# Performance work log

Measured on AMD Instinct MI355X. Metric: run time of the kernel, lower is better.

The kernel has to match this reference:

```python
import jax, jax.numpy as jnp
import numpy as np

N, E, C = 20000, 320000, 10000
IN, H, D = 768, 8, 64
HD = H * D
SA_H = 128


def _gat(feat, src, dst, W, al, ar, b):
    # DGL GATConv: fc -> per-node attn terms -> edge leaky_relu -> edge softmax over dst -> scatter-add -> bias -> elu
    h = (feat @ W).reshape(N, H, D)                       # [N,H,D]
    el = (h * al).sum(-1)                                 # [N,H]
    er = (h * ar).sum(-1)                                 # [N,H]
    e = jax.nn.leaky_relu(el[src] + er[dst], 0.2)         # [E,H]
    m = jax.ops.segment_max(e, dst, num_segments=N)       # [N,H]
    m = jnp.where(jnp.isfinite(m), m, 0.0)                # zero in-degree nodes
    ee = jnp.exp(e - m[dst])                              # [E,H]
    denom = jax.ops.segment_sum(ee, dst, num_segments=N)  # [N,H]
    a = ee / jnp.maximum(denom[dst], 1e-9)                # [E,H]
    out = jax.ops.segment_sum(a[:, :, None] * h[src], dst, num_segments=N)  # [N,H,D]
    return jax.nn.elu(out + b.reshape(1, H, D))


def _sem(z, w1, b1, w2):
    # SemanticAttention: per-metapath score -> softmax over metapaths -> weighted sum
    w = (jnp.tanh(z @ w1 + b1) @ w2).mean(0)              # [M,1]
    beta = jax.nn.softmax(w, axis=0)                      # [M,1]
    return (beta[None] * z).sum(1)                        # [C,HD]


def setup_inputs():
    key = jax.random.key(0)
    ks = jax.random.split(key, 32)
    inp = {}
    for i in range(3):
        inp[f"feat{i}"] = jax.random.normal(ks[i], (N, IN), jnp.float32)
        inp[f"src{i}"] = jax.random.randint(ks[3 + i], (E,), 0, N, dtype=jnp.int32)
        inp[f"dst{i}"] = jax.random.randint(ks[6 + i], (E,), 0, N, dtype=jnp.int32)
        inp[f"char{i}"] = jnp.arange(C, dtype=jnp.int32)
        inp[f"W{i}"] = jax.random.normal(ks[9 + i], (IN, HD), jnp.float32) * 0.05
        inp[f"al{i}"] = jax.random.normal(ks[12 + i], (H, D), jnp.float32) * 0.05
        inp[f"ar{i}"] = jax.random.normal(ks[15 + i], (H, D), jnp.float32) * 0.05
        inp[f"b{i}"] = jnp.zeros((HD,), jnp.float32)
    inp["sw1"] = jax.random.normal(ks[18], (HD, SA_H), jnp.float32) * 0.05
    inp["sb1"] = jnp.zeros((SA_H,), jnp.float32)
    inp["sw2"] = jax.random.normal(ks[19], (SA_H, 1), jnp.float32) * 0.05
    inp["aw1"] = jax.random.normal(ks[20], (HD, SA_H), jnp.float32) * 0.05
    inp["ab1"] = jnp.zeros((SA_H,), jnp.float32)
    inp["aw2"] = jax.random.normal(ks[21], (SA_H, 1), jnp.float32) * 0.05
    return inp


def reference(feat0, feat1, feat2, src0, src1, src2, dst0, dst1, dst2, char0, char1, char2,
              W0, W1, W2, al0, al1, al2, ar0, ar1, ar2, b0, b1, b2,
              sw1, sb1, sw2, aw1, ab1, aw2):
    h1 = _gat(feat0, src0, dst0, W0, al0, ar0, b0)        # [N,H,D]
    hh = _gat(feat2, src2, dst2, W2, al2, ar2, b2)        # [N,H,D]
    z = jnp.stack([h1[char0].reshape(C, HD), hh[char2].reshape(C, HD)], axis=1)  # [C,2,HD]
    sound = _sem(z, sw1, sb1, sw2)                        # [C,HD]
    h2 = _gat(feat1, src1, dst1, W1, al1, ar1, b1)        # [N,H,D]
    z2 = jnp.stack([sound, h2[char1].reshape(C, HD)], axis=1)  # [C,2,HD]
    sem_emb = _sem(z2, aw1, ab1, aw2).reshape(C, H, D)    # [C,H,D]
    h1 = h1.at[char0].set(sem_emb)
    h2 = h2.at[char1].set(sem_emb)
    hh = hh.at[char2].set(sem_emb)
    return sem_emb, h1.mean(1), h2.mean(1), hh.mean(1)
```

## Files before the change

kernel.cpp:

```cpp
#include <hip/hip_runtime.h>
#include <math.h>

#define NN 20000
#define NE 320000
#define CC 10000
#define KIN 768
#define NH 8
#define ND 64
#define NHD 512
#define NSA 128
#define NBKT 79

#define WTB_SZ (NHD * KIN)
#define W1TB_SZ (NSA * NHD)

typedef __attribute__((ext_vector_type(4))) float f32x4;
typedef __attribute__((ext_vector_type(8))) short s16x8;

__device__ __forceinline__ unsigned short f2bf(float f) {
  unsigned u = __float_as_uint(f);
  u += 0x7fffu + ((u >> 16) & 1u);
  return (unsigned short)(u >> 16);
}
__device__ __forceinline__ float bf2f(unsigned short s) {
  return __uint_as_float(((unsigned)s) << 16);
}
__device__ __forceinline__ float bflo(unsigned u) { return __uint_as_float(u << 16); }
__device__ __forceinline__ float bfhi(unsigned u) { return __uint_as_float(u & 0xffff0000u); }

__device__ __forceinline__ void gl_lds16(const void* g, void* l) {
  __builtin_amdgcn_global_load_lds(
      (const __attribute__((address_space(1))) unsigned int*)g,
      (__attribute__((address_space(3))) unsigned int*)l, 16, 0, 0);
}

__global__ void k_prep(const float* __restrict__ W0, const float* __restrict__ W1,
                       const float* __restrict__ W2, const float* __restrict__ sw1,
                       const float* __restrict__ aw1, unsigned short* __restrict__ wtb3,
                       unsigned short* __restrict__ w1tb2, int* __restrict__ deg3,
                       float* __restrict__ scal) {
  int i = blockIdx.x * 256 + threadIdx.x;
  if (i < 3 * WTB_SZ) {
    int g = i / WTB_SZ;
    int j = i - g * WTB_SZ;
    int n = j / KIN, k = j - n * KIN;
    const float* W = (g == 0) ? W0 : (g == 1) ? W1 : W2;
    wtb3[i] = f2bf(W[(size_t)k * NHD + n]);
    return;
  }
  i -= 3 * WTB_SZ;
  if (i < 2 * W1TB_SZ) {
    int p = i / W1TB_SZ;
    int j = i - p * W1TB_SZ;
    int n = j / NHD, k = j - n * NHD;
    const float* W = p ? aw1 : sw1;
    w1tb2[p * W1TB_SZ + n * NHD + k] = f2bf(W[(size_t)k * NSA + n]);
    return;
  }
  i -= 2 * W1TB_SZ;
  if (i < 3 * NN) { deg3[i] = 0; return; }
  i -= 3 * NN;
  if (i < 4) scal[i] = 0.f;
}

__global__ void k_cast_feat(const float* __restrict__ s, unsigned short* __restrict__ d, int n4) {
  int i = blockIdx.x * 256 + threadIdx.x;
  if (i >= n4) return;
  float4 v = ((const float4*)s)[i];
  ushort4 o;
  o.x = f2bf(v.x); o.y = f2bf(v.y); o.z = f2bf(v.z); o.w = f2bf(v.w);
  ((ushort4*)d)[i] = o;
}

template <int OUTBF>
__global__ __launch_bounds__(256, 2) void k_gemm(const unsigned short* __restrict__ A,
                                                 const unsigned short* __restrict__ Bt,
                                                 float* __restrict__ outf,
                                                 unsigned short* __restrict__ outb,
                                                 int M, int K, int ldc) {
  __shared__ unsigned short As[128 * 32];
  __shared__ unsigned short Bs[128 * 32];
  const int tid = threadIdx.x;
  const int wv = tid >> 6, lane = tid & 63;
  const int row0 = blockIdx.x * 128;
  const int col0 = blockIdx.y * 128;
  const int wr = (wv >> 1) * 64, wc = (wv & 1) * 64;
  const int ci = lane & 3, rsub = lane >> 2;

  f32x4 acc[4][4] = {};

  const int l15 = lane & 15;
  const int pc = (((lane >> 4) ^ ((l15 >> 1) & 3))) * 8;

  for (int k0 = 0; k0 < K; k0 += 32) {
#pragma unroll
    for (int i = 0; i < 2; i++) {
      int lrow = (wv * 2 + i) * 16 + rsub;
      int kc = (ci ^ ((lrow >> 1) & 3)) << 3;
      int ga = row0 + lrow; if (ga > M - 1) ga = M - 1;
      gl_lds16(A + (size_t)ga * K + k0 + kc, As + (wv * 2 + i) * 512);
      int gb = col0 + lrow;
      gl_lds16(Bt + (size_t)gb * K + k0 + kc, Bs + (wv * 2 + i) * 512);
    }
    __syncthreads();
    s16x8 af[4], bf[4];
#pragma unroll
    for (int m = 0; m < 4; m++) {
      af[m] = *(const s16x8*)(As + (wr + m * 16 + l15) * 32 + pc);
      bf[m] = *(const s16x8*)(Bs + (wc + m * 16 + l15) * 32 + pc);
    }
#pragma unroll
    for (int m = 0; m < 4; m++)
#pragma unroll
      for (int n = 0; n < 4; n++)
        acc[m][n] = __builtin_amdgcn_mfma_f32_16x16x32_bf16(af[m], bf[n], acc[m][n], 0, 0, 0);
    __syncthreads();
  }

  const int cbase = col0 + wc + l15;
  const int rq = (lane >> 4) * 4;
#pragma unroll
  for (int m = 0; m < 4; m++) {
#pragma unroll
    for (int r = 0; r < 4; r++) {
      int grow = row0 + wr + m * 16 + rq + r;
      if (grow < M) {
        if (OUTBF) {
          unsigned short* dp = outb + (size_t)grow * ldc + cbase;
#pragma unroll
          for (int n = 0; n < 4; n++) dp[n * 16] = f2bf(acc[m][n][r]);
        } else {
          float* dp = outf + (size_t)grow * ldc + cbase;
#pragma unroll
          for (int n = 0; n < 4; n++) dp[n * 16] = acc[m][n][r];
        }
      }
    }
  }
}

__global__ __launch_bounds__(256, 2) void k_gemm_sem(const unsigned short* __restrict__ A,
                                                     const unsigned short* __restrict__ Bt,
                                                     const float* __restrict__ b1,
                                                     const float* __restrict__ w2,
                                                     float* __restrict__ scal,
                                                     int M, int K) {
  __shared__ unsigned short As[128 * 32];
  __shared__ unsigned short Bs[128 * 32];
  __shared__ float rsum[2][128];
  __shared__ float pp[2][2];
  const int tid = threadIdx.x;
  const int wv = tid >> 6, lane = tid & 63;
  const int row0 = blockIdx.x * 128;
  const int wr = (wv >> 1) * 64, wc = (wv & 1) * 64;
  const int ci = lane & 3, rsub = lane >> 2;

  f32x4 acc[4][4] = {};

  const int l15 = lane & 15;
  const int pc = (((lane >> 4) ^ ((l15 >> 1) & 3))) * 8;

  for (int k0 = 0; k0 < K; k0 += 32) {
#pragma unroll
    for (int i = 0; i < 2; i++) {
      int lrow = (wv * 2 + i) * 16 + rsub;
      int kc = (ci ^ ((lrow >> 1) & 3)) << 3;
      int ga = row0 + lrow; if (ga > M - 1) ga = M - 1;
      gl_lds16(A + (size_t)ga * K + k0 + kc, As + (wv * 2 + i) * 512);
      int gb = lrow;
      gl_lds16(Bt + (size_t)gb * K + k0 + kc, Bs + (wv * 2 + i) * 512);
    }
    __syncthreads();
    s16x8 af[4], bf[4];
#pragma unroll
    for (int m = 0; m < 4; m++) {
      af[m] = *(const s16x8*)(As + (wr + m * 16 + l15) * 32 + pc);
      bf[m] = *(const s16x8*)(Bs + (wc + m * 16 + l15) * 32 + pc);
    }
#pragma unroll
    for (int m = 0; m < 4; m++)
#pragma unroll
      for (int n = 0; n < 4; n++)
        acc[m][n] = __builtin_amdgcn_mfma_f32_16x16x32_bf16(af[m], bf[n], acc[m][n], 0, 0, 0);
    __syncthreads();
  }

  if (tid < 128) { rsum[0][tid] = 0.f; rsum[1][tid] = 0.f; }
  __syncthreads();
  const int cb = wc + l15;
  const int rq = (lane >> 4) * 4;
  float b1c[4], w2c[4];
#pragma unroll
  for (int n = 0; n < 4; n++) { b1c[n] = b1[cb + n * 16]; w2c[n] = w2[cb + n * 16]; }
#pragma unroll
  for (int m = 0; m < 4; m++) {
#pragma unroll
    for (int r = 0; r < 4; r++) {
      int rl = wr + m * 16 + rq + r;
      float s = 0.f;
#pragma unroll
      for (int n = 0; n < 4; n++) s += tanhf(acc[m][n][r] + b1c[n]) * w2c[n];
      s += __shfl_xor(s, 1, 64); s += __shfl_xor(s, 2, 64);
      s += __shfl_xor(s, 4, 64); s += __shfl_xor(s, 8, 64);
      if (l15 == 0 && row0 + rl < M) rsum[wv & 1][rl] = s;
    }
  }
  __syncthreads();
  if (tid < 128) {
    int grow = row0 + tid;
    float v = rsum[0][tid] + rsum[1][tid];
    float vA = (grow < CC) ? v : 0.f;
    float vB = (grow >= CC && grow < M) ? v : 0.f;
#pragma unroll
    for (int off = 32; off > 0; off >>= 1) {
      vA += __shfl_xor(vA, off, 64);
      vB += __shfl_xor(vB, off, 64);
    }
    if ((tid & 63) == 0) { pp[tid >> 6][0] = vA; pp[tid >> 6][1] = vB; }
  }
  __syncthreads();
  if (tid == 0) {
    atomicAdd(scal + 0, pp[0][0] + pp[1][0]);
    atomicAdd(scal + 1, pp[0][1] + pp[1][1]);
  }
}

__global__ void k_elr(const unsigned short* __restrict__ hb, const float* __restrict__ al,
                      const float* __restrict__ ar, float* __restrict__ el,
                      float* __restrict__ er) {
  int t = (blockIdx.x * 256 + threadIdx.x) >> 6;
  int lane = threadIdx.x & 63;
  uint4 hv = *(const uint4*)(hb + (size_t)t * NHD + lane * 8);
  float4 al0 = ((const float4*)(al + lane * 8))[0];
  float4 al1 = ((const float4*)(al + lane * 8))[1];
  float4 ar0 = ((const float4*)(ar + lane * 8))[0];
  float4 ar1 = ((const float4*)(ar + lane * 8))[1];
  float h0 = bflo(hv.x), h1 = bfhi(hv.x), h2 = bflo(hv.y), h3 = bfhi(hv.y);
  float h4 = bflo(hv.z), h5 = bfhi(hv.z), h6 = bflo(hv.w), h7 = bfhi(hv.w);
  float a = h0 * al0.x + h1 * al0.y + h2 * al0.z + h3 * al0.w +
            h4 * al1.x + h5 * al1.y + h6 * al1.z + h7 * al1.w;
  float b = h0 * ar0.x + h1 * ar0.y + h2 * ar0.z + h3 * ar0.w +
            h4 * ar1.x + h5 * ar1.y + h6 * ar1.z + h7 * ar1.w;
#pragma unroll
  for (int off = 1; off < 8; off <<= 1) {
    a += __shfl_xor(a, off, 64);
    b += __shfl_xor(b, off, 64);
  }
  if ((lane & 7) == 0) {
    el[(size_t)t * NH + (lane >> 3)] = a;
    er[(size_t)t * NH + (lane >> 3)] = b;
  }
}

__global__ void k_hist3(const int* __restrict__ d0, const int* __restrict__ d1,
                        const int* __restrict__ d2, int* __restrict__ deg3) {
  int e = blockIdx.x * 256 + threadIdx.x;
  int g = blockIdx.y;
  const int* dst = (g == 0) ? d0 : (g == 1) ? d1 : d2;
  atomicAdd(deg3 + g * NN + dst[e], 1);
}

__global__ __launch_bounds__(1024) void k_scan3(const int* __restrict__ deg3,
                                                int* __restrict__ rowptr3,
                                                int* __restrict__ curB) {
  __shared__ int part[1024];
  const int g = blockIdx.x;
  const int* deg = deg3 + g * NN;
  int* rowptr = rowptr3 + g * (NN + 1);
  int tid = threadIdx.x;
  const int CH = 20;
  int base = tid * CH;
  int s = 0;
  for (int i = 0; i < CH; i++) { int idx = base + i; if (idx < NN) s += deg[idx]; }
  part[tid] = s;
  __syncthreads();
  for (int off = 1; off < 1024; off <<= 1) {
    int u = (tid >= off) ? part[tid - off] : 0;
    int v = part[tid];
    __syncthreads();
    part[tid] = u + v;
    __syncthreads();
  }
  int run = (tid == 0) ? 0 : part[tid - 1];
  for (int i = 0; i < CH; i++) {
    int idx = base + i;
    if (idx < NN) {
      rowptr[idx] = run;
      if ((idx & 255) == 0) curB[g * (NBKT + 1) + (idx >> 8)] = run;
      run += deg[idx];
    }
  }
  if (tid == 1023) rowptr[NN] = part[1023];
}

__global__ __launch_bounds__(1024) void k_coarse(const int* __restrict__ s0,
                                                 const int* __restrict__ s1,
                                                 const int* __restrict__ s2,
                                                 const int* __restrict__ d0,
                                                 const int* __restrict__ d1,
                                                 const int* __restrict__ d2,
                                                 int* __restrict__ curB,
                                                 unsigned* __restrict__ staging) {
  __shared__ int bcnt[NBKT];
  __shared__ int bbase[NBKT];
  int g = blockIdx.y;
  const int* src = (g == 0) ? s0 : (g == 1) ? s1 : s2;
  const int* dst = (g == 0) ? d0 : (g == 1) ? d1 : d2;
  int tid = threadIdx.x;
  if (tid < NBKT) bcnt[tid] = 0;
  __syncthreads();
  int e = blockIdx.x * 1024 + tid;
  bool val = e < NE;
  int b = 0, r = 0, sv = 0, dv = 0;
  if (val) {
    dv = dst[e]; sv = src[e];
    b = dv >> 8;
    r = atomicAdd(&bcnt[b], 1);
  }
  __syncthreads();
  if (tid < NBKT && bcnt[tid] > 0) bbase[tid] = atomicAdd(&curB[g * (NBKT + 1) + tid], bcnt[tid]);
  __syncthreads();
  if (val) staging[(size_t)g * NE + bbase[b] + r] = ((unsigned)sv << 8) | (unsigned)(dv & 255);
}

__global__ __launch_bounds__(1024) void k_fine(const int* __restrict__ rowptr3,
                                               const unsigned* __restrict__ staging,
                                               unsigned short* __restrict__ srcord3) {
  __shared__ int cur[256];
  int g = blockIdx.y, b = blockIdx.x;
  const int* rowptr = rowptr3 + g * (NN + 1);
  int n0 = b << 8;
  int tid = threadIdx.x;
  if (tid < 256) {
    int node = n0 + tid;
    cur[tid] = (node < NN) ? rowptr[node] : 0;
  }
  __syncthreads();
  int nend = n0 + 256; if (nend > NN) nend = NN;
  int start = rowptr[n0];
  int endp = rowptr[nend];
  for (int i = start + tid; i < endp; i += 1024) {
    unsigned u = staging[(size_t)g * NE + i];
    int nl = u & 255;
    int pos = atomicAdd(&cur[nl], 1);
    srcord3[(size_t)g * NE + pos] = (unsigned short)(u >> 8);
  }
}

__global__ __launch_bounds__(256) void k_aggf(const int* __restrict__ rowptr,
                                              const unsigned short* __restrict__ srcord,
                                              const float* __restrict__ el,
                                              const float* __restrict__ er,
                                              const unsigned short* __restrict__ hb,
                                              const float* __restrict__ bias,
                                              float* __restrict__ o,
                                              unsigned short* __restrict__ zb) {
  __shared__ float aS[4][64 * 8];
  __shared__ int sS[4][64];
  int wv = threadIdx.x >> 6;
  int t = (blockIdx.x * 256 + threadIdx.x) >> 6;
  int lane = threadIdx.x & 63;
  int h = lane >> 3;
  int beg = rowptr[t], end = rowptr[t + 1];

  float4 er0 = ((const float4*)(er + (size_t)t * NH))[0];
  float4 er1 = ((const float4*)(er + (size_t)t * NH))[1];
  float erow[8] = {er0.x, er0.y, er0.z, er0.w, er1.x, er1.y, er1.z, er1.w};

  float acc[8] = {0.f, 0.f, 0.f, 0.f, 0.f, 0.f, 0.f, 0.f};
  float den = 0.f;

  for (int cbeg = beg; cbeg < end; cbeg += 64) {
    int cnt = end - cbeg; if (cnt > 64) cnt = 64;
    bool valid = lane < cnt;
    int pidx = cbeg + lane; if (pidx > end - 1) pidx = end - 1;
    int s = srcord[pidx];
    if (valid) {
      sS[wv][lane] = s;
      float4 a0 = ((const float4*)(el + (size_t)s * NH))[0];
      float4 a1 = ((const float4*)(el + (size_t)s * NH))[1];
      float v[8] = {a0.x + erow[0], a0.y + erow[1], a0.z + erow[2], a0.w + erow[3],
                    a1.x + erow[4], a1.y + erow[5], a1.z + erow[6], a1.w + erow[7]};
#pragma unroll
      for (int k = 0; k < 8; k++) {
        float x = v[k];
        x = x >= 0.f ? x : 0.2f * x;
        aS[wv][lane * 8 + k] = expf(x);
      }
    }
    const unsigned short* hbl = hb + lane * 8;
    int q = 0;
    for (; q + 1 < cnt; q += 2) {
      int s0 = sS[wv][q], s1 = sS[wv][q + 1];
      float w0 = aS[wv][q * 8 + h];
      float w1 = aS[wv][(q + 1) * 8 + h];
      uint4 v0 = *(const uint4*)(hbl + (size_t)s0 * NHD);
      uint4 v1 = *(const uint4*)(hbl + (size_t)s1 * NHD);
      den += w0 + w1;
      acc[0] += w0 * bflo(v0.x); acc[1] += w0 * bfhi(v0.x);
      acc[2] += w0 * bflo(v0.y); acc[3] += w0 * bfhi(v0.y);
      acc[4] += w0 * bflo(v0.z); acc[5] += w0 * bfhi(v0.z);
      acc[6] += w0 * bflo(v0.w); acc[7] += w0 * bfhi(v0.w);
      acc[0] += w1 * bflo(v1.x); acc[1] += w1 * bfhi(v1.x);
      acc[2] += w1 * bflo(v1.y); acc[3] += w1 * bfhi(v1.y);
      acc[4] += w1 * bflo(v1.z); acc[5] += w1 * bfhi(v1.z);
      acc[6] += w1 * bflo(v1.w); acc[7] += w1 * bfhi(v1.w);
    }
    if (q < cnt) {
      int s0 = sS[wv][q];
      float w0 = aS[wv][q * 8 + h];
      uint4 v0 = *(const uint4*)(hbl + (size_t)s0 * NHD);
      den += w0;
      acc[0] += w0 * bflo(v0.x); acc[1] += w0 * bfhi(v0.x);
      acc[2] += w0 * bflo(v0.y); acc[3] += w0 * bfhi(v0.y);
      acc[4] += w0 * bflo(v0.z); acc[5] += w0 * bfhi(v0.z);
      acc[6] += w0 * bflo(v0.w); acc[7] += w0 * bfhi(v0.w);
    }
  }

  float dn = 1.f / fmaxf(den, 1e-9f);
  float4 b0 = ((const float4*)(bias + lane * 8))[0];
  float4 b1 = ((const float4*)(bias + lane * 8))[1];
  float r[8];
  r[0] = acc[0] * dn + b0.x; r[1] = acc[1] * dn + b0.y;
  r[2] = acc[2] * dn + b0.z; r[3] = acc[3] * dn + b0.w;
  r[4] = acc[4] * dn + b1.x; r[5] = acc[5] * dn + b1.y;
  r[6] = acc[6] * dn + b1.z; r[7] = acc[7] * dn + b1.w;
#pragma unroll
  for (int j = 0; j < 8; j++) r[j] = r[j] > 0.f ? r[j] : expm1f(r[j]);
  float* op = o + (size_t)t * NHD + lane * 8;
  ((float4*)op)[0] = make_float4(r[0], r[1], r[2], r[3]);
  ((float4*)op)[1] = make_float4(r[4], r[5], r[6], r[7]);
  if (t < CC) {
    uint4 z;
    z.x = ((unsigned)f2bf(r[1]) << 16) | f2bf(r[0]);
    z.y = ((unsigned)f2bf(r[3]) << 16) | f2bf(r[2]);
    z.z = ((unsigned)f2bf(r[5]) << 16) | f2bf(r[4]);
    z.w = ((unsigned)f2bf(r[7]) << 16) | f2bf(r[6]);
    *(uint4*)(zb + (size_t)t * NHD + lane * 8) = z;
  }
}

__global__ void k_combine_s1(const float* __restrict__ scal, const float* __restrict__ zA,
                             const float* __restrict__ zB, unsigned short* __restrict__ outb) {
  int i = blockIdx.x * 256 + threadIdx.x;
  float w0 = scal[0] * (1.f / CC), w1v = scal[1] * (1.f / CC);
  float mx = fmaxf(w0, w1v);
  float e0 = expf(w0 - mx), e1 = expf(w1v - mx);
  float inv = 1.f / (e0 + e1);
  float b0 = e0 * inv, b1v = e1 * inv;
  float4 a = ((const float4*)zA)[i];
  float4 b = ((const float4*)zB)[i];
  ushort4 z;
  z.x = f2bf(b0 * a.x + b1v * b.x);
  z.y = f2bf(b0 * a.y + b1v * b.y);
  z.z = f2bf(b0 * a.z + b1v * b.z);
  z.w = f2bf(b0 * a.w + b1v * b.w);
  ((ushort4*)outb)[i] = z;
}

__global__ void k_comb2_means(const float* __restrict__ scal,
                              const unsigned short* __restrict__ zsound,
                              const float* __restrict__ o0, const float* __restrict__ o1,
                              const float* __restrict__ o2, float* __restrict__ outf,
                              float* __restrict__ m1, float* __restrict__ m2,
                              float* __restrict__ m3) {
  int idx = blockIdx.x * 256 + threadIdx.x;
  int n = idx >> 6, d = idx & 63;
  if (n < CC) {
    float w0 = scal[0] * (1.f / CC), w1v = scal[1] * (1.f / CC);
    float mx = fmaxf(w0, w1v);
    float e0 = expf(w0 - mx), e1 = expf(w1v - mx);
    float inv = 1.f / (e0 + e1);
    float b0 = e0 * inv, b1v = e1 * inv;
    const unsigned short* zs = zsound + (size_t)n * NHD + d;
    const float* p1 = o1 + (size_t)n * NHD + d;
    float* po = outf + (size_t)n * NHD + d;
    float v = 0.f;
#pragma unroll
    for (int h = 0; h < 8; h++) {
      float r = b0 * bf2f(zs[h * 64]) + b1v * p1[h * 64];
      po[h * 64] = r;
      v += r;
    }
    v *= 0.125f;
    m1[idx] = v; m2[idx] = v; m3[idx] = v;
  } else {
    const float* p0 = o0 + (size_t)n * NHD + d;
    const float* p1 = o1 + (size_t)n * NHD + d;
    const float* p2 = o2 + (size_t)n * NHD + d;
    float v0 = 0.f, v1 = 0.f, v2 = 0.f;
#pragma unroll
    for (int h = 0; h < 8; h++) { v0 += p0[h * 64]; v1 += p1[h * 64]; v2 += p2[h * 64]; }
    m1[idx] = v0 * 0.125f; m2[idx] = v1 * 0.125f; m3[idx] = v2 * 0.125f;
  }
}

extern "C" void kernel_launch(void* const* d_in, const int* in_sizes, int n_in,
                              void* d_out, int out_size, void* d_ws, size_t ws_size,
                              hipStream_t stream) {
  (void)in_sizes; (void)n_in; (void)out_size; (void)ws_size;

  const float* feat[3]; const int* srcp[3]; const int* dstp[3];
  const float* Wp[3]; const float* alp[3]; const float* arp[3]; const float* bp[3];
  for (int g = 0; g < 3; g++) {
    const int base = g * 8;
    feat[g] = (const float*)d_in[base + 0];
    srcp[g] = (const int*)d_in[base + 1];
    dstp[g] = (const int*)d_in[base + 2];
    Wp[g]   = (const float*)d_in[base + 4];
    alp[g]  = (const float*)d_in[base + 5];
    arp[g]  = (const float*)d_in[base + 6];
    bp[g]   = (const float*)d_in[base + 7];
  }
  const float* sw1 = (const float*)d_in[24];
  const float* sb1 = (const float*)d_in[25];
  const float* sw2 = (const float*)d_in[26];
  const float* aw1 = (const float*)d_in[27];
  const float* ab1 = (const float*)d_in[28];
  const float* aw2 = (const float*)d_in[29];

  char* wsp = (char*)d_ws;
  auto alloc = [&](size_t bytes) {
    char* p = wsp;
    wsp += (bytes + 255) & ~(size_t)255;
    return p;
  };
  float* o0 = (float*)alloc((size_t)NN * NHD * 4);
  float* o1 = (float*)alloc((size_t)NN * NHD * 4);
  float* o2 = (float*)alloc((size_t)NN * NHD * 4);
  unsigned short* hb = (unsigned short*)alloc((size_t)NN * NHD * 2);
  unsigned short* featb = (unsigned short*)alloc((size_t)NN * KIN * 2);
  unsigned short* wtb3 = (unsigned short*)alloc((size_t)3 * WTB_SZ * 2);
  unsigned short* w1tb2 = (unsigned short*)alloc((size_t)2 * W1TB_SZ * 2);
  unsigned short* zcat = (unsigned short*)alloc((size_t)2 * CC * NHD * 2);
  float* el = (float*)alloc((size_t)NN * NH * 4);
  float* er = (float*)alloc((size_t)NN * NH * 4);
  float* scal = (float*)alloc(256);
  int* deg3 = (int*)alloc((size_t)3 * NN * 4);
  int* rowptr3 = (int*)alloc((size_t)3 * (NN + 1) * 4 + 64);
  int* curB = (int*)alloc((size_t)3 * (NBKT + 1) * 4);
  unsigned* staging = (unsigned*)alloc((size_t)3 * NE * 4);
  unsigned short* srcord3 = (unsigned short*)alloc((size_t)3 * NE * 2);

  float* outf = (float*)d_out;
  float* outm1 = outf + (size_t)CC * NHD;
  float* outm2 = outm1 + (size_t)NN * ND;
  float* outm3 = outm2 + (size_t)NN * ND;

  const int PREP_T = 3 * WTB_SZ + 2 * W1TB_SZ + 3 * NN + 4;
  k_prep<<<(PREP_T + 255) / 256, 256, 0, stream>>>(Wp[0], Wp[1], Wp[2], sw1, aw1,
                                                   wtb3, w1tb2, deg3, scal);
  k_hist3<<<dim3(NE / 256, 3), 256, 0, stream>>>(dstp[0], dstp[1], dstp[2], deg3);
  k_scan3<<<3, 1024, 0, stream>>>(deg3, rowptr3, curB);
  k_coarse<<<dim3((NE + 1023) / 1024, 3), 1024, 0, stream>>>(
      srcp[0], srcp[1], srcp[2], dstp[0], dstp[1], dstp[2], curB, staging);
  k_fine<<<dim3(NBKT, 3), 1024, 0, stream>>>(rowptr3, staging, srcord3);

  auto gat = [&](int g, float* og, unsigned short* zb) {
    k_cast_feat<<<NN * KIN / 4 / 256, 256, 0, stream>>>(feat[g], featb, NN * KIN / 4);
    k_gemm<1><<<dim3((NN + 127) / 128, NHD / 128), 256, 0, stream>>>(
        featb, wtb3 + (size_t)g * WTB_SZ, nullptr, hb, NN, KIN, NHD);
    k_elr<<<NN * 64 / 256, 256, 0, stream>>>(hb, alp[g], arp[g], el, er);
    k_aggf<<<NN * 64 / 256, 256, 0, stream>>>(rowptr3 + g * (NN + 1), srcord3 + (size_t)g * NE,
                                              el, er, hb, bp[g], og, zb);
  };

  gat(0, o0, zcat);
  gat(2, o2, zcat + (size_t)CC * NHD);

  k_gemm_sem<<<(2 * CC + 127) / 128, 256, 0, stream>>>(zcat, w1tb2, sb1, sw2, scal, 2 * CC, NHD);
  k_combine_s1<<<CC * NHD / 4 / 256, 256, 0, stream>>>(scal, o0, o2, zcat);

  gat(1, o1, zcat + (size_t)CC * NHD);

  k_gemm_sem<<<(2 * CC + 127) / 128, 256, 0, stream>>>(zcat, w1tb2 + W1TB_SZ, ab1, aw2,
                                                       scal + 2, 2 * CC, NHD);
  k_comb2_means<<<NN * 64 / 256, 256, 0, stream>>>(scal + 2, zcat, o0, o1, o2,
                                                   outf, outm1, outm2, outm3);
}
```

Before: 492.7 us.

## Fuse attention logits into GEMM epilogue and split aggregation per head

The GEMM epilogue now computes per-head el/er dot products with wave shuffles and writes them in a head-major layout, which removes the separate k_elr pass that re-read h. The aggregation kernel is restructured so each wave handles one (node, head) pair: it computes a single attention weight per edge and processes eight edges in parallel across lane groups, then reduces with shuffles. Blocks interleave heads so that gathers of the same source row are spread over eight blocks. This costs eight times more waves, repeated rowptr and srcord reads per head, and a cross-lane reduction at the end.

```diff
diff --git a/kernel.cpp b/kernel.cpp
--- a/kernel.cpp
+++ b/kernel.cpp
@@ -72,12 +72,13 @@
   ((ushort4*)d)[i] = o;
 }
 
-template <int OUTBF>
-__global__ __launch_bounds__(256, 2) void k_gemm(const unsigned short* __restrict__ A,
-                                                 const unsigned short* __restrict__ Bt,
-                                                 float* __restrict__ outf,
-                                                 unsigned short* __restrict__ outb,
-                                                 int M, int K, int ldc) {
+__global__ __launch_bounds__(256, 2) void k_gemm_gat(const unsigned short* __restrict__ A,
+                                                     const unsigned short* __restrict__ Bt,
+                                                     unsigned short* __restrict__ outb,
+                                                     const float* __restrict__ al,
+                                                     const float* __restrict__ ar,
+                                                     float* __restrict__ el_t,
+                                                     float* __restrict__ er_t) {
   __shared__ unsigned short As[128 * 32];
   __shared__ unsigned short Bs[128 * 32];
   const int tid = threadIdx.x;
@@ -92,15 +93,15 @@
   const int l15 = lane & 15;
   const int pc = (((lane >> 4) ^ ((l15 >> 1) & 3))) * 8;
 
-  for (int k0 = 0; k0 < K; k0 += 32) {
+  for (int k0 = 0; k0 < KIN; k0 += 32) {
 #pragma unroll
     for (int i = 0; i < 2; i++) {
       int lrow = (wv * 2 + i) * 16 + rsub;
       int kc = (ci ^ ((lrow >> 1) & 3)) << 3;
-      int ga = row0 + lrow; if (ga > M - 1) ga = M - 1;
-      gl_lds16(A + (size_t)ga * K + k0 + kc, As + (wv * 2 + i) * 512);
+      int ga = row0 + lrow; if (ga > NN - 1) ga = NN - 1;
+      gl_lds16(A + (size_t)ga * KIN + k0 + kc, As + (wv * 2 + i) * 512);
       int gb = col0 + lrow;
-      gl_lds16(Bt + (size_t)gb * K + k0 + kc, Bs + (wv * 2 + i) * 512);
+      gl_lds16(Bt + (size_t)gb * KIN + k0 + kc, Bs + (wv * 2 + i) * 512);
     }
     __syncthreads();
     s16x8 af[4], bf[4];
@@ -119,20 +120,34 @@
 
   const int cbase = col0 + wc + l15;
   const int rq = (lane >> 4) * 4;
+  const int hd = (col0 + wc) >> 6;
+  float alc[4], arc[4];
+#pragma unroll
+  for (int n = 0; n < 4; n++) { alc[n] = al[cbase + n * 16]; arc[n] = ar[cbase + n * 16]; }
+
 #pragma unroll
   for (int m = 0; m < 4; m++) {
 #pragma unroll
     for (int r = 0; r < 4; r++) {
       int grow = row0 + wr + m * 16 + rq + r;
-      if (grow < M) {
-        if (OUTBF) {
-          unsigned short* dp = outb + (size_t)grow * ldc + cbase;
-#pragma unroll
-          for (int n = 0; n < 4; n++) dp[n * 16] = f2bf(acc[m][n][r]);
-        } else {
-          float* dp = outf + (size_t)grow * ldc + cbase;
-#pragma unroll
-          for (int n = 0; n < 4; n++) dp[n * 16] = acc[m][n][r];
+      float a = 0.f, b = 0.f;
+#pragma unroll
+      for (int n = 0; n < 4; n++) {
+        float v = acc[m][n][r];
+        a += v * alc[n];
+        b += v * arc[n];
+      }
+      a += __shfl_xor(a, 1, 64); a += __shfl_xor(a, 2, 64);
+      a += __shfl_xor(a, 4, 64); a += __shfl_xor(a, 8, 64);
+      b += __shfl_xor(b, 1, 64); b += __shfl_xor(b, 2, 64);
+      b += __shfl_xor(b, 4, 64); b += __shfl_xor(b, 8, 64);
+      if (grow < NN) {
+        unsigned short* dp = outb + (size_t)grow * NHD + cbase;
+#pragma unroll
+        for (int n = 0; n < 4; n++) dp[n * 16] = f2bf(acc[m][n][r]);
+        if (l15 == 0) {
+          el_t[hd * NN + grow] = a;
+          er_t[hd * NN + grow] = b;
         }
       }
     }
@@ -225,33 +240,6 @@
   }
 }
 
-__global__ void k_elr(const unsigned short* __restrict__ hb, const float* __restrict__ al,
-                      const float* __restrict__ ar, float* __restrict__ el,
-                      float* __restrict__ er) {
-  int t = (blockIdx.x * 256 + threadIdx.x) >> 6;
-  int lane = threadIdx.x & 63;
-  uint4 hv = *(const uint4*)(hb + (size_t)t * NHD + lane * 8);
-  float4 al0 = ((const float4*)(al + lane * 8))[0];
-  float4 al1 = ((const float4*)(al + lane * 8))[1];
-  float4 ar0 = ((const float4*)(ar + lane * 8))[0];
-  float4 ar1 = ((const float4*)(ar + lane * 8))[1];
-  float h0 = bflo(hv.x), h1 = bfhi(hv.x), h2 = bflo(hv.y), h3 = bfhi(hv.y);
-  float h4 = bflo(hv.z), h5 = bfhi(hv.z), h6 = bflo(hv.w), h7 = bfhi(hv.w);
-  float a = h0 * al0.x + h1 * al0.y + h2 * al0.z + h3 * al0.w +
-            h4 * al1.x + h5 * al1.y + h6 * al1.z + h7 * al1.w;
-  float b = h0 * ar0.x + h1 * ar0.y + h2 * ar0.z + h3 * ar0.w +
-            h4 * ar1.x + h5 * ar1.y + h6 * ar1.z + h7 * ar1.w;
-#pragma unroll
-  for (int off = 1; off < 8; off <<= 1) {
-    a += __shfl_xor(a, off, 64);
-    b += __shfl_xor(b, off, 64);
-  }
-  if ((lane & 7) == 0) {
-    el[(size_t)t * NH + (lane >> 3)] = a;
-    er[(size_t)t * NH + (lane >> 3)] = b;
-  }
-}
-
 __global__ void k_hist3(const int* __restrict__ d0, const int* __restrict__ d1,
                         const int* __restrict__ d2, int* __restrict__ deg3) {
   int e = blockIdx.x * 256 + threadIdx.x;
@@ -347,97 +335,86 @@
   }
 }
 
-__global__ __launch_bounds__(256) void k_aggf(const int* __restrict__ rowptr,
+__global__ __launch_bounds__(256) void k_aggs(const int* __restrict__ rowptr,
                                               const unsigned short* __restrict__ srcord,
-                                              const float* __restrict__ el,
-                                              const float* __restrict__ er,
+                                              const float* __restrict__ el_t,
+                                              const float* __restrict__ er_t,
                                               const unsigned short* __restrict__ hb,
                                               const float* __restrict__ bias,
                                               float* __restrict__ o,
                                               unsigned short* __restrict__ zb) {
-  __shared__ float aS[4][64 * 8];
-  __shared__ int sS[4][64];
+  __shared__ float aS[4][64];
+  __shared__ unsigned short sS[4][64];
+  int bid = blockIdx.x;
+  int s = bid & 7;
   int wv = threadIdx.x >> 6;
-  int t = (blockIdx.x * 256 + threadIdx.x) >> 6;
+  int t = (bid >> 3) * 4 + wv;
   int lane = threadIdx.x & 63;
-  int h = lane >> 3;
+  int e8 = lane >> 3, c8 = lane & 7;
   int beg = rowptr[t], end = rowptr[t + 1];
-
-  float4 er0 = ((const float4*)(er + (size_t)t * NH))[0];
-  float4 er1 = ((const float4*)(er + (size_t)t * NH))[1];
-  float erow[8] = {er0.x, er0.y, er0.z, er0.w, er1.x, er1.y, er1.z, er1.w};
+  float ers = er_t[s * NN + t];
+  const float* els = el_t + s * NN;
 
   float acc[8] = {0.f, 0.f, 0.f, 0.f, 0.f, 0.f, 0.f, 0.f};
   float den = 0.f;
+  const unsigned short* hbs = hb + s * 64 + c8 * 8;
 
   for (int cbeg = beg; cbeg < end; cbeg += 64) {
     int cnt = end - cbeg; if (cnt > 64) cnt = 64;
-    bool valid = lane < cnt;
     int pidx = cbeg + lane; if (pidx > end - 1) pidx = end - 1;
-    int s = srcord[pidx];
-    if (valid) {
-      sS[wv][lane] = s;
-      float4 a0 = ((const float4*)(el + (size_t)s * NH))[0];
-      float4 a1 = ((const float4*)(el + (size_t)s * NH))[1];
-      float v[8] = {a0.x + erow[0], a0.y + erow[1], a0.z + erow[2], a0.w + erow[3],
-                    a1.x + erow[4], a1.y + erow[5], a1.z + erow[6], a1.w + erow[7]};
-#pragma unroll
-      for (int k = 0; k < 8; k++) {
-        float x = v[k];
-        x = x >= 0.f ? x : 0.2f * x;
-        aS[wv][lane * 8 + k] = expf(x);
-      }
-    }
-    const unsigned short* hbl = hb + lane * 8;
-    int q = 0;
-    for (; q + 1 < cnt; q += 2) {
-      int s0 = sS[wv][q], s1 = sS[wv][q + 1];
-      float w0 = aS[wv][q * 8 + h];
-      float w1 = aS[wv][(q + 1) * 8 + h];
-      uint4 v0 = *(const uint4*)(hbl + (size_t)s0 * NHD);
-      uint4 v1 = *(const uint4*)(hbl + (size_t)s1 * NHD);
-      den += w0 + w1;
-      acc[0] += w0 * bflo(v0.x); acc[1] += w0 * bfhi(v0.x);
-      acc[2] += w0 * bflo(v0.y); acc[3] += w0 * bfhi(v0.y);
-      acc[4] += w0 * bflo(v0.z); acc[5] += w0 * bfhi(v0.z);
-      acc[6] += w0 * bflo(v0.w); acc[7] += w0 * bfhi(v0.w);
-      acc[0] += w1 * bflo(v1.x); acc[1] += w1 * bfhi(v1.x);
-      acc[2] += w1 * bflo(v1.y); acc[3] += w1 * bfhi(v1.y);
-      acc[4] += w1 * bflo(v1.z); acc[5] += w1 * bfhi(v1.z);
-      acc[6] += w1 * bflo(v1.w); acc[7] += w1 * bfhi(v1.w);
-    }
-    if (q < cnt) {
-      int s0 = sS[wv][q];
-      float w0 = aS[wv][q * 8 + h];
-      uint4 v0 = *(const uint4*)(hbl + (size_t)s0 * NHD);
-      den += w0;
-      acc[0] += w0 * bflo(v0.x); acc[1] += w0 * bfhi(v0.x);
-      acc[2] += w0 * bflo(v0.y); acc[3] += w0 * bfhi(v0.y);
-      acc[4] += w0 * bflo(v0.z); acc[5] += w0 * bfhi(v0.z);
-      acc[6] += w0 * bflo(v0.w); acc[7] += w0 * bfhi(v0.w);
-    }
-  }
-
-  float dn = 1.f / fmaxf(den, 1e-9f);
-  float4 b0 = ((const float4*)(bias + lane * 8))[0];
-  float4 b1 = ((const float4*)(bias + lane * 8))[1];
-  float r[8];
-  r[0] = acc[0] * dn + b0.x; r[1] = acc[1] * dn + b0.y;
-  r[2] = acc[2] * dn + b0.z; r[3] = acc[3] * dn + b0.w;
-  r[4] = acc[4] * dn + b1.x; r[5] = acc[5] * dn + b1.y;
-  r[6] = acc[6] * dn + b1.z; r[7] = acc[7] * dn + b1.w;
-#pragma unroll
-  for (int j = 0; j < 8; j++) r[j] = r[j] > 0.f ? r[j] : expm1f(r[j]);
-  float* op = o + (size_t)t * NHD + lane * 8;
-  ((float4*)op)[0] = make_float4(r[0], r[1], r[2], r[3]);
-  ((float4*)op)[1] = make_float4(r[4], r[5], r[6], r[7]);
-  if (t < CC) {
-    uint4 z;
-    z.x = ((unsigned)f2bf(r[1]) << 16) | f2bf(r[0]);
-    z.y = ((unsigned)f2bf(r[3]) << 16) | f2bf(r[2]);
-    z.z = ((unsigned)f2bf(r[5]) << 16) | f2bf(r[4]);
-    z.w = ((unsigned)f2bf(r[7]) << 16) | f2bf(r[6]);
-    *(uint4*)(zb + (size_t)t * NHD + lane * 8) = z;
+    int sv = srcord[pidx];
+    sS[wv][lane] = (unsigned short)sv;
+    float w = 0.f;
+    if (lane < cnt) {
+      float x = els[sv] + ers;
+      x = x >= 0.f ? x : 0.2f * x;
+      w = __expf(x);
+    }
+    aS[wv][lane] = w;
+    int iters = (cnt + 7) >> 3;
+    for (int it = 0; it < iters; it++) {
+      int q = it * 8 + e8;
+      float wq = aS[wv][q];
+      int sq = sS[wv][q];
+      uint4 v = *(const uint4*)(hbs + (size_t)sq * NHD);
+      den += wq;
+      acc[0] += wq * bflo(v.x); acc[1] += wq * bfhi(v.x);
+      acc[2] += wq * bflo(v.y); acc[3] += wq * bfhi(v.y);
+      acc[4] += wq * bflo(v.z); acc[5] += wq * bfhi(v.z);
+      acc[6] += wq * bflo(v.w); acc[7] += wq * bfhi(v.w);
+    }
+  }
+
+#pragma unroll
+  for (int off = 8; off < 64; off <<= 1) {
+    den += __shfl_xor(den, off, 64);
+#pragma unroll
+    for (int j = 0; j < 8; j++) acc[j] += __shfl_xor(acc[j], off, 64);
+  }
+
+  if (e8 == 0) {
+    float dn = 1.f / fmaxf(den, 1e-9f);
+    int colb = s * 64 + c8 * 8;
+    float4 b0 = ((const float4*)(bias + colb))[0];
+    float4 b1 = ((const float4*)(bias + colb))[1];
+    float r[8];
+    r[0] = acc[0] * dn + b0.x; r[1] = acc[1] * dn + b0.y;
+    r[2] = acc[2] * dn + b0.z; r[3] = acc[3] * dn + b0.w;
+    r[4] = acc[4] * dn + b1.x; r[5] = acc[5] * dn + b1.y;
+    r[6] = acc[6] * dn + b1.z; r[7] = acc[7] * dn + b1.w;
+#pragma unroll
+    for (int j = 0; j < 8; j++) r[j] = r[j] > 0.f ? r[j] : expm1f(r[j]);
+    float* op = o + (size_t)t * NHD + colb;
+    ((float4*)op)[0] = make_float4(r[0], r[1], r[2], r[3]);
+    ((float4*)op)[1] = make_float4(r[4], r[5], r[6], r[7]);
+    if (t < CC) {
+      uint4 z;
+      z.x = ((unsigned)f2bf(r[1]) << 16) | f2bf(r[0]);
+      z.y = ((unsigned)f2bf(r[3]) << 16) | f2bf(r[2]);
+      z.z = ((unsigned)f2bf(r[5]) << 16) | f2bf(r[4]);
+      z.w = ((unsigned)f2bf(r[7]) << 16) | f2bf(r[6]);
+      *(uint4*)(zb + (size_t)t * NHD + colb) = z;
+    }
   }
 }
 
@@ -534,8 +511,8 @@
   unsigned short* wtb3 = (unsigned short*)alloc((size_t)3 * WTB_SZ * 2);
   unsigned short* w1tb2 = (unsigned short*)alloc((size_t)2 * W1TB_SZ * 2);
   unsigned short* zcat = (unsigned short*)alloc((size_t)2 * CC * NHD * 2);
-  float* el = (float*)alloc((size_t)NN * NH * 4);
-  float* er = (float*)alloc((size_t)NN * NH * 4);
+  float* el_t = (float*)alloc((size_t)NN * NH * 4);
+  float* er_t = (float*)alloc((size_t)NN * NH * 4);
   float* scal = (float*)alloc(256);
   int* deg3 = (int*)alloc((size_t)3 * NN * 4);
   int* rowptr3 = (int*)alloc((size_t)3 * (NN + 1) * 4 + 64);
@@ -559,11 +536,10 @@
 
   auto gat = [&](int g, float* og, unsigned short* zb) {
     k_cast_feat<<<NN * KIN / 4 / 256, 256, 0, stream>>>(feat[g], featb, NN * KIN / 4);
-    k_gemm<1><<<dim3((NN + 127) / 128, NHD / 128), 256, 0, stream>>>(
-        featb, wtb3 + (size_t)g * WTB_SZ, nullptr, hb, NN, KIN, NHD);
-    k_elr<<<NN * 64 / 256, 256, 0, stream>>>(hb, alp[g], arp[g], el, er);
-    k_aggf<<<NN * 64 / 256, 256, 0, stream>>>(rowptr3 + g * (NN + 1), srcord3 + (size_t)g * NE,
-                                              el, er, hb, bp[g], og, zb);
+    k_gemm_gat<<<dim3((NN + 127) / 128, NHD / 128), 256, 0, stream>>>(
+        featb, wtb3 + (size_t)g * WTB_SZ, hb, alp[g], arp[g], el_t, er_t);
+    k_aggs<<<NN * 8 / 4, 256, 0, stream>>>(rowptr3 + g * (NN + 1), srcord3 + (size_t)g * NE,
+                                           el_t, er_t, hb, bp[g], og, zb);
   };
 
   gat(0, o0, zcat);
```

Measured after the change: 582.4 us. 1.18x slower.
